# Performance work log

Hardware: AMD Instinct MI355X
Metric: run time of the kernel (lower is better)

Reference implementation:

```python
import jax, jax.numpy as jnp
import numpy as np

B, S, D, H = 4, 2048, 1024, 16
DH = D // H
EPS = 1e-12  # F.normalize default eps
MIN_TEMP = 0.01


def setup_inputs() -> dict:
    key = jax.random.key(0)
    ks = jax.random.split(key, 8)
    lim = 1.0 / np.sqrt(DH)  # torch Linear init bound
    return {
        "sequences": jax.random.normal(ks[0], (B, S, D), dtype=jnp.float32),
        "Wq": jax.random.uniform(ks[1], (H, DH, DH), jnp.float32, -lim, lim),
        "bq": jax.random.uniform(ks[2], (H, DH), jnp.float32, -lim, lim),
        "Wk": jax.random.uniform(ks[3], (H, DH, DH), jnp.float32, -lim, lim),
        "bk": jax.random.uniform(ks[4], (H, DH), jnp.float32, -lim, lim),
        "Wv": jax.random.uniform(ks[5], (H, DH, DH), jnp.float32, -lim, lim),
        "bv": jax.random.uniform(ks[6], (H, DH), jnp.float32, -lim, lim),
        "temp": jnp.ones((H,), dtype=jnp.float32),
    }


def _l2norm(x):
    n = jnp.linalg.norm(x, axis=-1, keepdims=True)
    return x / jnp.maximum(n, EPS)


def reference(sequences, Wq, bq, Wk, bk, Wv, bv, temp):
    # split channels into heads: [B, S, H, DH]
    x = sequences.reshape(B, S, H, DH)
    # per-head Linear: y = x @ W.T + b  (W is [out, in])
    q = jnp.einsum("bshd,hed->bshe", x, Wq) + bq
    k = jnp.einsum("bshd,hed->bshe", x, Wk) + bk
    v = jnp.einsum("bshd,hed->bshe", x, Wv) + bv
    # cosine attention with learned per-head temperature
    q = _l2norm(q)
    k = _l2norm(k)
    scale = jnp.maximum(temp, MIN_TEMP)  # clamp_min(0.01)
    logits = jnp.einsum("bshe,bthe->bhst", q, k) * scale[None, :, None, None]
    attn = jax.nn.softmax(logits, axis=-1)
    # dropout is identity in eval / deterministic reference
    out = jnp.einsum("bhst,bthe->bshe", attn, v)
    return out.reshape(B, S, D)
```

## Files before the change

kernel.cpp:

```cpp
#include <hip/hip_runtime.h>
#include <hip/hip_bf16.h>

#define B_ 4
#define S_ 2048
#define D_ 1024
#define H_ 16
#define DH_ 64
#define QBLK 128
#define KVBLK 64
#define NT (S_ / KVBLK)
#define EPS_ 1e-12f
#define LOG2E_ 1.44269504f

typedef __attribute__((ext_vector_type(8))) short bf16x8;
typedef __attribute__((ext_vector_type(4))) float f32x4;

static __device__ __forceinline__ unsigned short f2bf(float f) {
    __hip_bfloat16 h = __float2bfloat16(f);
    return *reinterpret_cast<unsigned short*>(&h);
}

static __device__ __forceinline__ float fast_exp2(float x) {
#if __has_builtin(__builtin_amdgcn_exp2f)
    return __builtin_amdgcn_exp2f(x);
#else
    return exp2f(x);
#endif
}

static __device__ __forceinline__ unsigned int cvt_pk_bf16(float lo, float hi) {
    unsigned int r;
    asm("v_cvt_pk_bf16_f32 %0, %1, %2" : "=v"(r) : "v"(lo), "v"(hi));
    return r;
}

static __device__ __forceinline__ int swz(int row, int chunk) {
    return (row << 6) + ((chunk ^ (row & 7)) << 3);
}

static __device__ __forceinline__ int kperm(int kk) {
    return ((kk & 4) << 2) | ((kk >> 1) & 12) | (kk & 3);
}

__global__ __launch_bounds__(256) void wcast_kernel(
    const float* __restrict__ Wq, const float* __restrict__ Wk,
    const float* __restrict__ Wv, unsigned short* __restrict__ wbf)
{
    const int idx = blockIdx.x * 256 + threadIdx.x;
    const int i = idx * 4;
    const int mat = i >> 16;
    const int off = i & 65535;
    const float* src = (mat == 0) ? Wq : (mat == 1) ? Wk : Wv;
    float4 v = *reinterpret_cast<const float4*>(src + off);
    ushort4 o;
    o.x = f2bf(v.x); o.y = f2bf(v.y); o.z = f2bf(v.z); o.w = f2bf(v.w);
    *reinterpret_cast<ushort4*>(wbf + i) = o;
}

__global__ __launch_bounds__(256) void proj_kernel(
    const float* __restrict__ x, const unsigned short* __restrict__ wbf,
    const float* __restrict__ bq, const float* __restrict__ bk,
    const float* __restrict__ bv, const float* __restrict__ temp,
    unsigned short* __restrict__ q_ws, unsigned short* __restrict__ k_ws,
    unsigned short* __restrict__ v_ws)
{
    __shared__ unsigned short x_lds[64][72];
    __shared__ unsigned short vt_lds[64][72];

    const int h    = blockIdx.y;
    const int tok0 = blockIdx.x * 64;
    const int b    = tok0 >> 11;
    const int s0   = tok0 & (S_ - 1);
    const int bh   = b * H_ + h;
    const int t    = threadIdx.x;
    const int wave = t >> 6, lane = t & 63, c = lane & 15, g = lane >> 4;

    {
        const int row = t >> 2, seg = t & 3;
        const float* xp = x + (size_t)(tok0 + row) * D_ + h * DH_ + seg * 16;
#pragma unroll
        for (int i = 0; i < 4; ++i) {
            float4 v = *reinterpret_cast<const float4*>(xp + i * 4);
            ushort4 o;
            o.x = f2bf(v.x); o.y = f2bf(v.y); o.z = f2bf(v.z); o.w = f2bf(v.w);
            *reinterpret_cast<ushort4*>(&x_lds[row][seg * 16 + i * 4]) = o;
        }
    }
    __syncthreads();

    bf16x8 a0 = *reinterpret_cast<const bf16x8*>(&x_lds[wave * 16 + c][g * 8]);
    bf16x8 a1 = *reinterpret_cast<const bf16x8*>(&x_lds[wave * 16 + c][32 + g * 8]);

    const float scaleq = fmaxf(temp[h], 0.01f) * LOG2E_;

#pragma unroll
    for (int mat = 0; mat < 3; ++mat) {
        const unsigned short* wb = wbf + mat * (H_ * DH_ * DH_) + h * (DH_ * DH_);
        const float* bias = ((mat == 0) ? bq : (mat == 1) ? bk : bv) + h * DH_;

        f32x4 acc[4];
#pragma unroll
        for (int m = 0; m < 4; ++m) acc[m] = (f32x4){0.f, 0.f, 0.f, 0.f};
#pragma unroll
        for (int m = 0; m < 4; ++m) {
            bf16x8 b0 = *reinterpret_cast<const bf16x8*>(wb + (m * 16 + c) * DH_ + g * 8);
            bf16x8 b1 = *reinterpret_cast<const bf16x8*>(wb + (m * 16 + c) * DH_ + 32 + g * 8);
            acc[m] = __builtin_amdgcn_mfma_f32_16x16x32_bf16(a0, b0, acc[m], 0, 0, 0);
            acc[m] = __builtin_amdgcn_mfma_f32_16x16x32_bf16(a1, b1, acc[m], 0, 0, 0);
        }
#pragma unroll
        for (int m = 0; m < 4; ++m) {
            float bm = bias[m * 16 + c];
#pragma unroll
            for (int j = 0; j < 4; ++j) acc[m][j] += bm;
        }

        if (mat < 2) {
            float rinv[4];
            const float sc = (mat == 0) ? scaleq : 1.0f;
#pragma unroll
            for (int j = 0; j < 4; ++j) {
                float p = acc[0][j] * acc[0][j] + acc[1][j] * acc[1][j] +
                          acc[2][j] * acc[2][j] + acc[3][j] * acc[3][j];
                p += __shfl_xor(p, 1); p += __shfl_xor(p, 2);
                p += __shfl_xor(p, 4); p += __shfl_xor(p, 8);
                rinv[j] = sc / fmaxf(sqrtf(p), EPS_);
            }
            unsigned short* dst = (mat == 0) ? q_ws : k_ws;
#pragma unroll
            for (int m = 0; m < 4; ++m)
#pragma unroll
                for (int j = 0; j < 4; ++j) {
                    int sl = wave * 16 + 4 * g + j;
                    int row = (mat == 1) ? ((sl & ~31) | kperm(sl & 31)) : sl;
                    dst[((size_t)bh * S_ + s0 + row) * DH_ + m * 16 + c] =
                        f2bf(acc[m][j] * rinv[j]);
                }
        } else {
#pragma unroll
            for (int m = 0; m < 4; ++m) {
                ushort4 o;
                o.x = f2bf(acc[m][0]); o.y = f2bf(acc[m][1]);
                o.z = f2bf(acc[m][2]); o.w = f2bf(acc[m][3]);
                *reinterpret_cast<ushort4*>(&vt_lds[m * 16 + c][wave * 16 + 4 * g]) = o;
            }
        }
    }
    __syncthreads();

    {
        const int e = t >> 2, ch = t & 3;
        bf16x8 v0 = *reinterpret_cast<const bf16x8*>(&vt_lds[e][ch * 16]);
        bf16x8 v1 = *reinterpret_cast<const bf16x8*>(&vt_lds[e][ch * 16 + 8]);
        unsigned short* vp = v_ws + ((size_t)bh * DH_ + e) * S_ + s0 + ch * 16;
        *reinterpret_cast<bf16x8*>(vp) = v0;
        *reinterpret_cast<bf16x8*>(vp + 8) = v1;
    }
}

__global__ __launch_bounds__(256, 4) void attn_kernel(
    const unsigned short* __restrict__ q_ws, const unsigned short* __restrict__ k_ws,
    const unsigned short* __restrict__ v_ws, float* __restrict__ out)
{
    __shared__ unsigned short K_lds[2][64 * 64];
    __shared__ unsigned short V_lds[2][64 * 64];

    const int nwg = gridDim.x;
    const int w   = (blockIdx.x & 7) * (nwg >> 3) + (blockIdx.x >> 3);
    const int qt  = w & 15;
    const int bh  = w >> 4;

    const int t = threadIdx.x;
    const int lane = t & 63, c = lane & 15, g = lane >> 4;
    const int wave = t >> 6;
    const int qrow0 = qt * QBLK + wave * 32;

    const unsigned short* qbase = q_ws + (size_t)bh * S_ * DH_;
    const unsigned short* kbase = k_ws + (size_t)bh * S_ * DH_;
    const unsigned short* vbase = v_ws + (size_t)bh * DH_ * S_;

    bf16x8 qa[2][2];
#pragma unroll
    for (int qi = 0; qi < 2; ++qi)
#pragma unroll
        for (int kd = 0; kd < 2; ++kd)
            qa[qi][kd] = *reinterpret_cast<const bf16x8*>(
                qbase + (size_t)(qrow0 + qi * 16 + c) * DH_ + kd * 32 + g * 8);

    const int srow = t >> 2, sch = (t & 3) * 2;
    bf16x8 kr0, kr1, vr0, vr1;
    auto load_tile = [&](int kt) {
        const unsigned short* kp = kbase + (size_t)(kt * KVBLK + srow) * DH_ + sch * 8;
        kr0 = *reinterpret_cast<const bf16x8*>(kp);
        kr1 = *reinterpret_cast<const bf16x8*>(kp + 8);
        const unsigned short* vp = vbase + (size_t)srow * S_ + kt * KVBLK + sch * 8;
        vr0 = *reinterpret_cast<const bf16x8*>(vp);
        vr1 = *reinterpret_cast<const bf16x8*>(vp + 8);
    };
    auto store_tile = [&](int buf) {
        *reinterpret_cast<bf16x8*>(&K_lds[buf][swz(srow, sch)])     = kr0;
        *reinterpret_cast<bf16x8*>(&K_lds[buf][swz(srow, sch + 1)]) = kr1;
        *reinterpret_cast<bf16x8*>(&V_lds[buf][swz(srow, sch)])     = vr0;
        *reinterpret_cast<bf16x8*>(&V_lds[buf][swz(srow, sch + 1)]) = vr1;
    };

    load_tile(0);
    store_tile(0);
    __syncthreads();

    f32x4 o[2][4];
    float l[2] = {0.f, 0.f};
#pragma unroll
    for (int qi = 0; qi < 2; ++qi)
#pragma unroll
        for (int m = 0; m < 4; ++m) o[qi][m] = (f32x4){0.f, 0.f, 0.f, 0.f};

    for (int kt = 0; kt < NT; ++kt) {
        const int cur = kt & 1;
        const bool more = (kt + 1 < NT);
        if (more) load_tile(kt + 1);

        const unsigned short* Kb = &K_lds[cur][0];
        const unsigned short* Vb = &V_lds[cur][0];

#pragma unroll
        for (int ks = 0; ks < 2; ++ks) {
            f32x4 s[2][2];
#pragma unroll
            for (int nn = 0; nn < 2; ++nn) {
                const int krow = ks * 32 + nn * 16 + c;
                bf16x8 a0 = *reinterpret_cast<const bf16x8*>(&Kb[swz(krow, g)]);
                bf16x8 a1 = *reinterpret_cast<const bf16x8*>(&Kb[swz(krow, 4 + g)]);
#pragma unroll
                for (int qi = 0; qi < 2; ++qi) {
                    f32x4 acc = (f32x4){0.f, 0.f, 0.f, 0.f};
                    acc = __builtin_amdgcn_mfma_f32_16x16x32_bf16(a0, qa[qi][0], acc, 0, 0, 0);
                    acc = __builtin_amdgcn_mfma_f32_16x16x32_bf16(a1, qa[qi][1], acc, 0, 0, 0);
                    s[qi][nn] = acc;
                }
            }

            bf16x8 pa[2];
#pragma unroll
            for (int qi = 0; qi < 2; ++qi) {
                float p0 = fast_exp2(s[qi][0][0]), p1 = fast_exp2(s[qi][0][1]);
                float p2 = fast_exp2(s[qi][0][2]), p3 = fast_exp2(s[qi][0][3]);
                float p4 = fast_exp2(s[qi][1][0]), p5 = fast_exp2(s[qi][1][1]);
                float p6 = fast_exp2(s[qi][1][2]), p7 = fast_exp2(s[qi][1][3]);
                l[qi] += ((p0 + p1) + (p2 + p3)) + ((p4 + p5) + (p6 + p7));
                union { unsigned int u[4]; bf16x8 v; } pk;
                pk.u[0] = cvt_pk_bf16(p0, p1);
                pk.u[1] = cvt_pk_bf16(p2, p3);
                pk.u[2] = cvt_pk_bf16(p4, p5);
                pk.u[3] = cvt_pk_bf16(p6, p7);
                pa[qi] = pk.v;
            }

#pragma unroll
            for (int m = 0; m < 4; ++m) {
                bf16x8 vb = *reinterpret_cast<const bf16x8*>(&Vb[swz(m * 16 + c, ks * 4 + g)]);
                o[0][m] = __builtin_amdgcn_mfma_f32_16x16x32_bf16(pa[0], vb, o[0][m], 0, 0, 0);
                o[1][m] = __builtin_amdgcn_mfma_f32_16x16x32_bf16(pa[1], vb, o[1][m], 0, 0, 0);
            }
        }

        if (more) store_tile(cur ^ 1);
        __syncthreads();
    }

    float rl[2];
#pragma unroll
    for (int qi = 0; qi < 2; ++qi) {
        float v = l[qi];
        v += __shfl_xor(v, 16);
        v += __shfl_xor(v, 32);
        rl[qi] = v;
    }

    const int bb = bh >> 4, hh = bh & 15;
#pragma unroll
    for (int qi = 0; qi < 2; ++qi)
#pragma unroll
        for (int j = 0; j < 4; ++j) {
            float inv = 1.0f / __shfl(rl[qi], 4 * g + j);
            const int srow_ = qrow0 + qi * 16 + 4 * g + j;
            float* op = out + (size_t)(bb * S_ + srow_) * D_ + hh * DH_;
#pragma unroll
            for (int m = 0; m < 4; ++m)
                op[m * 16 + c] = o[qi][m][j] * inv;
        }
}

extern "C" void kernel_launch(void* const* d_in, const int* in_sizes, int n_in,
                              void* d_out, int out_size, void* d_ws, size_t ws_size,
                              hipStream_t stream) {
    const float* x    = (const float*)d_in[0];
    const float* Wq   = (const float*)d_in[1];
    const float* bq   = (const float*)d_in[2];
    const float* Wk   = (const float*)d_in[3];
    const float* bk   = (const float*)d_in[4];
    const float* Wv   = (const float*)d_in[5];
    const float* bv   = (const float*)d_in[6];
    const float* temp = (const float*)d_in[7];
    float* out = (float*)d_out;

    const size_t QKV_ELEMS = (size_t)B_ * H_ * S_ * DH_;
    unsigned short* q_ws = (unsigned short*)d_ws;
    unsigned short* k_ws = q_ws + QKV_ELEMS;
    unsigned short* v_ws = k_ws + QKV_ELEMS;

    unsigned short* wbf = (unsigned short*)d_out;

    wcast_kernel<<<192, 256, 0, stream>>>(Wq, Wk, Wv, wbf);

    dim3 gp(B_ * S_ / 64, H_);
    proj_kernel<<<gp, 256, 0, stream>>>(x, wbf, bq, bk, bv, temp, q_ws, k_ws, v_ws);

    dim3 ga(B_ * H_ * (S_ / QBLK));
    attn_kernel<<<ga, 256, 0, stream>>>(q_ws, k_ws, v_ws, out);
}
```

Baseline: 115.2 us.

## Split attention work across 8 waves with 16 query rows each

The attention kernel moves from 4 waves handling 32 query rows each to 8 waves handling 16 rows each, with 512 threads per block. Each thread now loads one K and one V chunk per tile instead of two. The aim is more waves to hide latency and fewer registers per thread. In exchange, each K/V fragment read from LDS is reused by half as many MFMAs, which raises LDS traffic. s_setprio is also added around the compute section to favor MFMA-issuing waves.

```diff
diff --git a/kernel.cpp b/kernel.cpp
--- a/kernel.cpp
+++ b/kernel.cpp
@@ -158,7 +158,7 @@
     }
 }
 
-__global__ __launch_bounds__(256, 4) void attn_kernel(
+__global__ __launch_bounds__(512, 8) void attn_kernel(
     const unsigned short* __restrict__ q_ws, const unsigned short* __restrict__ k_ws,
     const unsigned short* __restrict__ v_ws, float* __restrict__ out)
 {
@@ -173,47 +173,39 @@
     const int t = threadIdx.x;
     const int lane = t & 63, c = lane & 15, g = lane >> 4;
     const int wave = t >> 6;
-    const int qrow0 = qt * QBLK + wave * 32;
+    const int qrow0 = qt * QBLK + wave * 16;
 
     const unsigned short* qbase = q_ws + (size_t)bh * S_ * DH_;
     const unsigned short* kbase = k_ws + (size_t)bh * S_ * DH_;
     const unsigned short* vbase = v_ws + (size_t)bh * DH_ * S_;
 
-    bf16x8 qa[2][2];
-#pragma unroll
-    for (int qi = 0; qi < 2; ++qi)
-#pragma unroll
-        for (int kd = 0; kd < 2; ++kd)
-            qa[qi][kd] = *reinterpret_cast<const bf16x8*>(
-                qbase + (size_t)(qrow0 + qi * 16 + c) * DH_ + kd * 32 + g * 8);
-
-    const int srow = t >> 2, sch = (t & 3) * 2;
-    bf16x8 kr0, kr1, vr0, vr1;
+    bf16x8 qa[2];
+#pragma unroll
+    for (int kd = 0; kd < 2; ++kd)
+        qa[kd] = *reinterpret_cast<const bf16x8*>(
+            qbase + (size_t)(qrow0 + c) * DH_ + kd * 32 + g * 8);
+
+    const int srow = t >> 3, sch = t & 7;
+    bf16x8 kr, vr;
     auto load_tile = [&](int kt) {
-        const unsigned short* kp = kbase + (size_t)(kt * KVBLK + srow) * DH_ + sch * 8;
-        kr0 = *reinterpret_cast<const bf16x8*>(kp);
-        kr1 = *reinterpret_cast<const bf16x8*>(kp + 8);
-        const unsigned short* vp = vbase + (size_t)srow * S_ + kt * KVBLK + sch * 8;
-        vr0 = *reinterpret_cast<const bf16x8*>(vp);
-        vr1 = *reinterpret_cast<const bf16x8*>(vp + 8);
+        kr = *reinterpret_cast<const bf16x8*>(
+            kbase + (size_t)(kt * KVBLK + srow) * DH_ + sch * 8);
+        vr = *reinterpret_cast<const bf16x8*>(
+            vbase + (size_t)srow * S_ + kt * KVBLK + sch * 8);
     };
     auto store_tile = [&](int buf) {
-        *reinterpret_cast<bf16x8*>(&K_lds[buf][swz(srow, sch)])     = kr0;
-        *reinterpret_cast<bf16x8*>(&K_lds[buf][swz(srow, sch + 1)]) = kr1;
-        *reinterpret_cast<bf16x8*>(&V_lds[buf][swz(srow, sch)])     = vr0;
-        *reinterpret_cast<bf16x8*>(&V_lds[buf][swz(srow, sch + 1)]) = vr1;
+        *reinterpret_cast<bf16x8*>(&K_lds[buf][swz(srow, sch)]) = kr;
+        *reinterpret_cast<bf16x8*>(&V_lds[buf][swz(srow, sch)]) = vr;
     };
 
     load_tile(0);
     store_tile(0);
     __syncthreads();
 
-    f32x4 o[2][4];
-    float l[2] = {0.f, 0.f};
-#pragma unroll
-    for (int qi = 0; qi < 2; ++qi)
-#pragma unroll
-        for (int m = 0; m < 4; ++m) o[qi][m] = (f32x4){0.f, 0.f, 0.f, 0.f};
+    f32x4 o[4];
+    float l = 0.f;
+#pragma unroll
+    for (int m = 0; m < 4; ++m) o[m] = (f32x4){0.f, 0.f, 0.f, 0.f};
 
     for (int kt = 0; kt < NT; ++kt) {
         const int cur = kt & 1;
@@ -223,72 +215,59 @@
         const unsigned short* Kb = &K_lds[cur][0];
         const unsigned short* Vb = &V_lds[cur][0];
 
+        __builtin_amdgcn_s_setprio(1);
 #pragma unroll
         for (int ks = 0; ks < 2; ++ks) {
-            f32x4 s[2][2];
+            f32x4 s[2];
 #pragma unroll
             for (int nn = 0; nn < 2; ++nn) {
                 const int krow = ks * 32 + nn * 16 + c;
                 bf16x8 a0 = *reinterpret_cast<const bf16x8*>(&Kb[swz(krow, g)]);
                 bf16x8 a1 = *reinterpret_cast<const bf16x8*>(&Kb[swz(krow, 4 + g)]);
-#pragma unroll
-                for (int qi = 0; qi < 2; ++qi) {
-                    f32x4 acc = (f32x4){0.f, 0.f, 0.f, 0.f};
-                    acc = __builtin_amdgcn_mfma_f32_16x16x32_bf16(a0, qa[qi][0], acc, 0, 0, 0);
-                    acc = __builtin_amdgcn_mfma_f32_16x16x32_bf16(a1, qa[qi][1], acc, 0, 0, 0);
-                    s[qi][nn] = acc;
-                }
+                f32x4 acc = (f32x4){0.f, 0.f, 0.f, 0.f};
+                acc = __builtin_amdgcn_mfma_f32_16x16x32_bf16(a0, qa[0], acc, 0, 0, 0);
+                acc = __builtin_amdgcn_mfma_f32_16x16x32_bf16(a1, qa[1], acc, 0, 0, 0);
+                s[nn] = acc;
             }
 
-            bf16x8 pa[2];
-#pragma unroll
-            for (int qi = 0; qi < 2; ++qi) {
-                float p0 = fast_exp2(s[qi][0][0]), p1 = fast_exp2(s[qi][0][1]);
-                float p2 = fast_exp2(s[qi][0][2]), p3 = fast_exp2(s[qi][0][3]);
-                float p4 = fast_exp2(s[qi][1][0]), p5 = fast_exp2(s[qi][1][1]);
-                float p6 = fast_exp2(s[qi][1][2]), p7 = fast_exp2(s[qi][1][3]);
-                l[qi] += ((p0 + p1) + (p2 + p3)) + ((p4 + p5) + (p6 + p7));
-                union { unsigned int u[4]; bf16x8 v; } pk;
-                pk.u[0] = cvt_pk_bf16(p0, p1);
-                pk.u[1] = cvt_pk_bf16(p2, p3);
-                pk.u[2] = cvt_pk_bf16(p4, p5);
-                pk.u[3] = cvt_pk_bf16(p6, p7);
-                pa[qi] = pk.v;
-            }
+            float p0 = fast_exp2(s[0][0]), p1 = fast_exp2(s[0][1]);
+            float p2 = fast_exp2(s[0][2]), p3 = fast_exp2(s[0][3]);
+            float p4 = fast_exp2(s[1][0]), p5 = fast_exp2(s[1][1]);
+            float p6 = fast_exp2(s[1][2]), p7 = fast_exp2(s[1][3]);
+            l += ((p0 + p1) + (p2 + p3)) + ((p4 + p5) + (p6 + p7));
+            union { unsigned int u[4]; bf16x8 v; } pk;
+            pk.u[0] = cvt_pk_bf16(p0, p1);
+            pk.u[1] = cvt_pk_bf16(p2, p3);
+            pk.u[2] = cvt_pk_bf16(p4, p5);
+            pk.u[3] = cvt_pk_bf16(p6, p7);
+            bf16x8 pa = pk.v;
 
 #pragma unroll
             for (int m = 0; m < 4; ++m) {
                 bf16x8 vb = *reinterpret_cast<const bf16x8*>(&Vb[swz(m * 16 + c, ks * 4 + g)]);
-                o[0][m] = __builtin_amdgcn_mfma_f32_16x16x32_bf16(pa[0], vb, o[0][m], 0, 0, 0);
-                o[1][m] = __builtin_amdgcn_mfma_f32_16x16x32_bf16(pa[1], vb, o[1][m], 0, 0, 0);
+                o[m] = __builtin_amdgcn_mfma_f32_16x16x32_bf16(pa, vb, o[m], 0, 0, 0);
             }
         }
+        __builtin_amdgcn_s_setprio(0);
 
         if (more) store_tile(cur ^ 1);
         __syncthreads();
     }
 
-    float rl[2];
-#pragma unroll
-    for (int qi = 0; qi < 2; ++qi) {
-        float v = l[qi];
-        v += __shfl_xor(v, 16);
-        v += __shfl_xor(v, 32);
-        rl[qi] = v;
-    }
+    float rl = l;
+    rl += __shfl_xor(rl, 16);
+    rl += __shfl_xor(rl, 32);
 
     const int bb = bh >> 4, hh = bh & 15;
 #pragma unroll
-    for (int qi = 0; qi < 2; ++qi)
-#pragma unroll
-        for (int j = 0; j < 4; ++j) {
-            float inv = 1.0f / __shfl(rl[qi], 4 * g + j);
-            const int srow_ = qrow0 + qi * 16 + 4 * g + j;
-            float* op = out + (size_t)(bb * S_ + srow_) * D_ + hh * DH_;
-#pragma unroll
-            for (int m = 0; m < 4; ++m)
-                op[m * 16 + c] = o[qi][m][j] * inv;
-        }
+    for (int j = 0; j < 4; ++j) {
+        float inv = 1.0f / __shfl(rl, 4 * g + j);
+        const int srw = qrow0 + 4 * g + j;
+        float* op = out + (size_t)(bb * S_ + srw) * D_ + hh * DH_;
+#pragma unroll
+        for (int m = 0; m < 4; ++m)
+            op[m * 16 + c] = o[m][j] * inv;
+    }
 }
 
 extern "C" void kernel_launch(void* const* d_in, const int* in_sizes, int n_in,
@@ -317,5 +296,5 @@
     proj_kernel<<<gp, 256, 0, stream>>>(x, wbf, bq, bk, bv, temp, q_ws, k_ws, v_ws);
 
     dim3 ga(B_ * H_ * (S_ / QBLK));
-    attn_kernel<<<ga, 256, 0, stream>>>(q_ws, k_ws, v_ws, out);
-}
+    attn_kernel<<<ga, 512, 0, stream>>>(q_ws, k_ws, v_ws, out);
+}
```

New measurement: 117.7 us. +2.2%, slower.
